# Kernel tuning notes

Measured on AMD Instinct MI355X. Metric: run time of the kernel, lower is better.

## Reference

```python
import jax, jax.numpy as jnp
import numpy as np

N = 20
DM = 128
C_CLIP = 10.0
BATCH = 16384


def setup_inputs() -> dict:
    key = jax.random.key(0)
    ks = jax.random.split(key, 9)
    s = 1.0 / np.sqrt(DM)
    inp = {
        "x": jax.random.normal(ks[0], (BATCH, N, DM), dtype=jnp.float32),
        "Wg": jax.random.uniform(ks[1], (DM, DM), jnp.float32, -s, s),
        "bg": jax.random.uniform(ks[2], (DM,), jnp.float32, -s, s),
        "Wn": jax.random.uniform(ks[3], (DM, DM), jnp.float32, -s, s),
        "bn": jax.random.uniform(ks[4], (DM,), jnp.float32, -s, s),
        "Wk": jax.random.uniform(ks[5], (DM, DM), jnp.float32, -s, s),
        "bk": jax.random.uniform(ks[6], (DM,), jnp.float32, -s, s),
        "Wq": jax.random.uniform(ks[7], (DM, DM), jnp.float32, -s, s),
        "bq": jax.random.uniform(ks[8], (DM,), jnp.float32, -s, s),
    }
    return inp


def reference(x, Wg, bg, Wn, bn, Wk, bk, Wq, bq):
    B, n, dm = x.shape
    # graph embedding: max-pool over nodes
    x_graph = jnp.max(x, axis=1)                      # [B, dm]
    lp_graph = x_graph @ Wg.T + bg                    # [B, dm]
    lp_nodes = x @ Wn.T + bn                          # [B, n, dm]
    h = lp_nodes + lp_graph[:, None, :]               # [B, n, dm]
    K = h @ Wk.T + bk                                 # [B, n, dm]
    Q = h @ Wq.T + bq                                 # [B, n, dm]
    M = jnp.einsum("bnd,bmd->bnm", K, Q) / np.float32(np.sqrt(dm))
    M_hat = C_CLIP * jnp.tanh(M) - jnp.eye(n, dtype=M.dtype) * 1e20
    # flattened (global) softmax over all n*n entries
    p = jax.nn.softmax(M_hat.reshape(B, n * n), axis=1)
    return p.reshape(B, n, n)
```

## Files before the change

kernel.cpp:

```cpp
#include <hip/hip_runtime.h>
#include <hip/hip_bf16.h>
#include <math.h>

#define DM 128
#define NN 20
#define NB 16384
#define BPB 8

#define OFF_A      0
#define OFF_AT     16384
#define OFF_WA     32768
#define OFF_WAT    49152
#define OFF_AG     65536
#define OFF_BMAT   81920
#define OFF_S1T    98304
#define OFF_S2T    114688
#define OFF_C2T    131072
#define OFF_U0     147456
#define OFF_V0     147584
#define OFF_T0     147712
#define OFF_W1     147840
#define OFF_AT0    147968
#define OFF_A0     148096
#define OFF_B0     148224
#define OFF_C1     148352
#define OFF_C00    148480
#define OFF_CBASE  148481
#define OFF_FRAGB  149504
#define OFF_FRAGS  (149504 + 8192)

#define INVS 0.08838834764831845f

typedef _Float16 h16;
typedef h16 half8 __attribute__((ext_vector_type(8)));
typedef h16 half4v __attribute__((ext_vector_type(4)));
typedef h16 half2v __attribute__((ext_vector_type(2)));
typedef float f32x4 __attribute__((ext_vector_type(4)));
typedef unsigned int uint4v __attribute__((ext_vector_type(4)));

#define MFMA16(a, b, c) __builtin_amdgcn_mfma_f32_16x16x32_f16((a), (b), (c), 0, 0, 0)

__device__ __forceinline__ int swz(int row, int col) {
    return (row * 128 + col) ^ ((row & 7) << 3);
}

__device__ __forceinline__ unsigned pkmax(unsigned a, unsigned b) {
    const half2v r = __builtin_elementwise_max(__builtin_bit_cast(half2v, a),
                                               __builtin_bit_cast(half2v, b));
    return __builtin_bit_cast(unsigned, r);
}

__device__ __forceinline__ unsigned pk2(float a, float b) {
    const half2v p = { (h16)a, (h16)b };
    return __builtin_bit_cast(unsigned, p);
}

__device__ __forceinline__ int fb_idx(int k, int j) {
    return ((j >> 4) << 11) | ((k >> 5) << 9)
         | ((((k >> 3) & 3) * 16 + (j & 15)) << 3) | (k & 7);
}

__global__ void k_prep1(const float* __restrict__ Wk, const float* __restrict__ Wq,
                        const float* __restrict__ bk, const float* __restrict__ bq,
                        const float* __restrict__ bn, const float* __restrict__ bg,
                        float* __restrict__ ws) {
    const int bx = blockIdx.x, t = threadIdx.x;
    __shared__ float sbuf[128];
    if (bx < 128) {
        sbuf[t] = Wk[t * 128 + bx];
        __syncthreads();
        float a = 0.f;
        #pragma unroll 8
        for (int d = 0; d < 128; ++d) a += sbuf[d] * Wq[d * 128 + t];
        ws[OFF_A  + bx * 128 + t] = a;
        ws[OFF_AT + t * 128 + bx] = a;
    } else {
        float u = 0.f, v = 0.f;
        #pragma unroll 8
        for (int d = 0; d < 128; ++d) {
            u += Wk[d * 128 + t] * bq[d];
            v += Wq[d * 128 + t] * bk[d];
        }
        ws[OFF_U0 + t] = u;
        ws[OFF_V0 + t] = v;
        ws[OFF_T0 + t] = bn[t] + bg[t];
        sbuf[t] = bk[t] * bq[t];
        __syncthreads();
        for (int s = 64; s > 0; s >>= 1) { if (t < s) sbuf[t] += sbuf[t + s]; __syncthreads(); }
        if (t == 0) ws[OFF_C00] = sbuf[0];
    }
}

__global__ void k_prep2(const float* __restrict__ Wn, const float* __restrict__ Wg,
                        float* __restrict__ ws) {
    const int bx = blockIdx.x, t = threadIdx.x;
    __shared__ float s1[128], s2[128];
    if (bx < 128) {
        const int r = bx;
        s1[t] = Wn[t * 128 + r];
        s2[t] = ws[OFF_A + r * 128 + t];
        __syncthreads();
        float wa = 0.f, wat = 0.f, ag = 0.f;
        #pragma unroll 4
        for (int e = 0; e < 128; ++e) {
            wa  += s1[e] * ws[OFF_A  + e * 128 + t];
            wat += s1[e] * ws[OFF_AT + e * 128 + t];
            ag  += s2[e] * Wg[e * 128 + t];
        }
        ws[OFF_WA  + r * 128 + t] = wa;
        ws[OFF_WAT + r * 128 + t] = wat;
        ws[OFF_AG  + r * 128 + t] = ag;
    } else {
        const float t0t = ws[OFF_T0 + t], u0t = ws[OFF_U0 + t], v0t = ws[OFF_V0 + t];
        float w1 = 0.f, at0 = 0.f;
        #pragma unroll 8
        for (int e = 0; e < 128; ++e) {
            const float t0e = ws[OFF_T0 + e];
            w1  += (ws[OFF_A + t * 128 + e] + ws[OFF_AT + t * 128 + e]) * t0e;
            at0 +=  ws[OFF_A + t * 128 + e] * t0e;
        }
        w1 += u0t + v0t;
        ws[OFF_W1  + t] = w1;
        ws[OFF_AT0 + t] = at0;
        s1[t] = t0t * (at0 + u0t + v0t);
        __syncthreads();
        for (int s = 64; s > 0; s >>= 1) { if (t < s) s1[t] += s1[t + s]; __syncthreads(); }
        if (t == 0) ws[OFF_CBASE] = s1[0] + ws[OFF_C00];
    }
}

__global__ void k_prep3(const float* __restrict__ Wn, const float* __restrict__ Wg,
                        float* __restrict__ ws) {
    const int bx = blockIdx.x, t = threadIdx.x;
    __shared__ float wa[128], wat[128], wgc[128];
    h16* fB = (h16*)(ws + OFF_FRAGB);
    h16* fS = (h16*)(ws + OFF_FRAGS);
    if (bx < 128) {
        const int r = bx;
        wa[t]  = ws[OFF_WA  + r * 128 + t];
        wat[t] = ws[OFF_WAT + r * 128 + t];
        wgc[t] = Wg[t * 128 + r];
        __syncthreads();
        float bm = 0.f, s1v = 0.f, s2v = 0.f, c2v = 0.f;
        #pragma unroll 4
        for (int f = 0; f < 128; ++f) {
            bm  += wa[f]  * Wn[f * 128 + t];
            s1v += wa[f]  * Wg[f * 128 + t];
            s2v += wat[f] * Wg[f * 128 + t];
            c2v += wgc[f] * ws[OFF_AG + f * 128 + t];
        }
        fB[fb_idx(r, t)]       = (h16)bm;
        fS[fb_idx(t, r)]       = (h16)s1v;
        fS[fb_idx(t, r + 128)] = (h16)s2v;
        fS[fb_idx(t, r + 256)] = (h16)c2v;
    } else {
        float a0 = 0.f, b0 = 0.f, c1 = 0.f;
        #pragma unroll 8
        for (int f = 0; f < 128; ++f) {
            a0 += ws[OFF_WA  + t * 128 + f] * ws[OFF_T0 + f] + Wn[f * 128 + t] * ws[OFF_U0 + f];
            b0 += ws[OFF_WAT + t * 128 + f] * ws[OFF_T0 + f] + Wn[f * 128 + t] * ws[OFF_V0 + f];
            c1 += Wg[f * 128 + t] * ws[OFF_W1 + f];
        }
        ws[OFF_A0 + t] = a0;
        ws[OFF_B0 + t] = b0;
        ws[OFF_C1 + t] = c1;
    }
}

__global__ __launch_bounds__(512, 4) void k_fused(const float* __restrict__ x,
                                                  const float* __restrict__ ws,
                                                  float* __restrict__ out) {
    __shared__ __align__(16) h16 xgl[BPB * 128];
    __shared__ __align__(16) h16 avhL[BPB * 2 * 128];
    __shared__ float abL[BPB][40];
    __shared__ float cpart[BPB][BPB];
    __shared__ float cbs[BPB];

    const int t = threadIdx.x, l = t & 63, w = t >> 6;
    const int lc = l & 15, lg = l >> 4;
    const int b = blockIdx.x * BPB + w;
    const half8 h8z = {};

    const float* xb = x + (size_t)b * 2560;
    half8 xa0[4], xa1[4];
    #pragma unroll
    for (int ks = 0; ks < 4; ++ks) {
        const float4 v0 = *(const float4*)(xb + lc * 128 + 32 * ks + 8 * lg);
        const float4 v1 = *(const float4*)(xb + lc * 128 + 32 * ks + 8 * lg + 4);
        xa0[ks] = (half8){ (h16)v0.x, (h16)v0.y, (h16)v0.z, (h16)v0.w,
                           (h16)v1.x, (h16)v1.y, (h16)v1.z, (h16)v1.w };
    }
    #pragma unroll
    for (int ks = 0; ks < 4; ++ks) {
        half8 v = h8z;
        if (lc < 4) {
            const float4 v0 = *(const float4*)(xb + (16 + lc) * 128 + 32 * ks + 8 * lg);
            const float4 v1 = *(const float4*)(xb + (16 + lc) * 128 + 32 * ks + 8 * lg + 4);
            v = (half8){ (h16)v0.x, (h16)v0.y, (h16)v0.z, (h16)v0.w,
                         (h16)v1.x, (h16)v1.y, (h16)v1.z, (h16)v1.w };
        }
        xa1[ks] = v;
    }

    #pragma unroll
    for (int ks = 0; ks < 4; ++ks) {
        uint4v m0 = __builtin_bit_cast(uint4v, xa0[ks]);
        uint4v m1 = __builtin_bit_cast(uint4v, xa1[ks]);
        #pragma unroll
        for (int s = 1; s < 16; s <<= 1) {
            #pragma unroll
            for (int wd = 0; wd < 4; ++wd)
                m0[wd] = pkmax(m0[wd], (unsigned)__shfl_xor((int)m0[wd], s));
        }
        #pragma unroll
        for (int s = 1; s < 4; s <<= 1) {
            #pragma unroll
            for (int wd = 0; wd < 4; ++wd)
                m1[wd] = pkmax(m1[wd], (unsigned)__shfl_xor((int)m1[wd], s));
        }
        #pragma unroll
        for (int wd = 0; wd < 4; ++wd) {
            const unsigned m1b = (unsigned)__shfl((int)m1[wd], l & 51);
            m0[wd] = pkmax(m0[wd], m1b);
        }
        if (lc == 0)
            *(half8*)(xgl + swz(w, 32 * ks + 8 * lg)) = __builtin_bit_cast(half8, m0);
    }
    __syncthreads();

    {
        const half8* fS = (const half8*)(ws + OFF_FRAGS);
        f32x4 sacc[3];
        #pragma unroll
        for (int i = 0; i < 3; ++i) sacc[i] = (f32x4){0.f, 0.f, 0.f, 0.f};
        #pragma unroll
        for (int ks = 0; ks < 4; ++ks) {
            const half8 ag = *(const half8*)(xgl + swz(lc & 7, 32 * ks + 8 * lg));
            #pragma unroll
            for (int i = 0; i < 3; ++i) {
                const int ct = w + 8 * i;
                sacc[i] = MFMA16(ag, fS[(ct * 4 + ks) * 64 + l], sacc[i]);
            }
        }
        #pragma unroll
        for (int i = 0; i < 2; ++i) {
            const int ct = w + 8 * i;
            const int v = ct >> 3, c128 = 16 * (ct & 7) + lc;
            const float bias = (v == 0) ? ws[OFF_A0 + c128] : ws[OFF_B0 + c128];
            if (lg < 2) {
                #pragma unroll
                for (int r = 0; r < 4; ++r)
                    avhL[(4 * lg + r) * 256 + v * 128 + c128] = (h16)(sacc[i][r] + bias);
            }
        }
        {
            const int j = 16 * w + lc;
            const float c1j = ws[OFF_C1 + j];
            float p[4];
            #pragma unroll
            for (int r = 0; r < 4; ++r) {
                const float xgv = (float)xgl[swz((4 * lg + r) & 7, j)];
                p[r] = (sacc[2][r] + c1j) * xgv;
            }
            #pragma unroll
            for (int r = 0; r < 4; ++r) {
                float v = p[r];
                v += __shfl_xor(v, 1); v += __shfl_xor(v, 2);
                v += __shfl_xor(v, 4); v += __shfl_xor(v, 8);
                if (lc == 0 && lg < 2) cpart[4 * lg + r][w] = v;
            }
        }
    }
    __syncthreads();
    if (t < BPB) {
        float s = ws[OFF_CBASE];
        #pragma unroll
        for (int j = 0; j < BPB; ++j) s += cpart[t][j];
        cbs[t] = s;
    }
    __syncthreads();

    half8 s8[4];
    #pragma unroll
    for (int ks = 0; ks < 4; ++ks) {
        half8 v = h8z;
        if (lc < 2) v = *(const half8*)(avhL + w * 256 + lc * 128 + 32 * ks + 8 * lg);
        s8[ks] = v;
    }
    {
        f32x4 a0c = {0.f, 0.f, 0.f, 0.f}, a1c = {0.f, 0.f, 0.f, 0.f};
        #pragma unroll
        for (int ks = 0; ks < 4; ++ks) {
            a0c = MFMA16(xa0[ks], s8[ks], a0c);
            a1c = MFMA16(xa1[ks], s8[ks], a1c);
        }
        if (lc == 0) {
            #pragma unroll
            for (int r = 0; r < 4; ++r) abL[w][4 * lg + r] = a0c[r];
            if (lg == 0) {
                #pragma unroll
                for (int r = 0; r < 4; ++r) abL[w][16 + r] = a1c[r];
            }
        }
        if (lc == 1) {
            #pragma unroll
            for (int r = 0; r < 4; ++r) abL[w][20 + 4 * lg + r] = a0c[r];
            if (lg == 0) {
                #pragma unroll
                for (int r = 0; r < 4; ++r) abL[w][36 + r] = a1c[r];
            }
        }
    }

    const half8* fB = (const half8*)(ws + OFF_FRAGB);
    f32x4 macc[2][2];
    #pragma unroll
    for (int mt = 0; mt < 2; ++mt)
        #pragma unroll
        for (int ctn = 0; ctn < 2; ++ctn) macc[mt][ctn] = (f32x4){0.f, 0.f, 0.f, 0.f};
    const bool hs = (l < 32);
    const int s1 = lc + ((l >> 4) & 1) * 32;
    const int s2 = s1 + 16;
    #pragma unroll
    for (int km = 0; km < 4; ++km) {
        unsigned P[2][2][2];
        #pragma unroll
        for (int rp = 0; rp < 2; ++rp) {
            const int rt = 2 * km + rp;
            f32x4 f0 = {0.f, 0.f, 0.f, 0.f}, f1 = {0.f, 0.f, 0.f, 0.f};
            #pragma unroll
            for (int ks = 0; ks < 4; ++ks) {
                const half8 a = fB[(rt * 4 + ks) * 64 + l];
                f0 = MFMA16(a, xa0[ks], f0);
                f1 = MFMA16(a, xa1[ks], f1);
            }
            P[rp][0][0] = pk2(f0[0], f0[1]); P[rp][0][1] = pk2(f0[2], f0[3]);
            P[rp][1][0] = pk2(f1[0], f1[1]); P[rp][1][1] = pk2(f1[2], f1[3]);
        }
        #pragma unroll
        for (int ctn = 0; ctn < 2; ++ctn) {
            const unsigned A0 = (unsigned)__shfl((int)P[0][ctn][0], s1);
            const unsigned B0 = (unsigned)__shfl((int)P[1][ctn][0], s1);
            const unsigned A1 = (unsigned)__shfl((int)P[0][ctn][1], s1);
            const unsigned B1 = (unsigned)__shfl((int)P[1][ctn][1], s1);
            const unsigned A2 = (unsigned)__shfl((int)P[0][ctn][0], s2);
            const unsigned B2 = (unsigned)__shfl((int)P[1][ctn][0], s2);
            const unsigned A3 = (unsigned)__shfl((int)P[0][ctn][1], s2);
            const unsigned B3 = (unsigned)__shfl((int)P[1][ctn][1], s2);
            const uint4v uu = { hs ? A0 : B0, hs ? A1 : B1,
                                hs ? A2 : B2, hs ? A3 : B3 };
            const half8 bX = __builtin_bit_cast(half8, uu);
            macc[0][ctn] = MFMA16(xa0[km], bX, macc[0][ctn]);
            macc[1][ctn] = MFMA16(xa1[km], bX, macc[1][ctn]);
        }
    }
    asm volatile("s_waitcnt lgkmcnt(0)" ::: "memory");

    const float cb = cbs[w];
    const float an0 = abL[w][lc];
    const float an1 = (lc < 4) ? abL[w][16 + lc] : 0.f;
    float bmv0[4], bmv1[4];
    #pragma unroll
    for (int r = 0; r < 4; ++r) {
        bmv0[r] = abL[w][20 + 4 * lg + r];
        bmv1[r] = (lg == 0) ? abL[w][36 + r] : 0.f;
    }
    float pv[2][2][4];
    float psum = 0.f;
    #pragma unroll
    for (int mt = 0; mt < 2; ++mt) {
        #pragma unroll
        for (int ctn = 0; ctn < 2; ++ctn) {
            #pragma unroll
            for (int r = 0; r < 4; ++r) {
                const int n = 16 * ctn + lc;
                const int m = 16 * mt + 4 * lg + r;
                const bool valid = (ctn == 0 || lc < 4) && (mt == 0 || lg == 0) && (n != m);
                const float Mv = (macc[mt][ctn][r] + (ctn ? an1 : an0)
                                  + (mt ? bmv1[r] : bmv0[r]) + cb) * INVS;
                const float E = __expf(2.f * Mv);
                const float e = valid ? __expf(-20.f / (E + 1.f)) : 0.f;
                pv[mt][ctn][r] = e;
                psum += e;
            }
        }
    }
    #pragma unroll
    for (int off = 32; off > 0; off >>= 1) psum += __shfl_xor(psum, off);
    const float inv = 1.f / psum;

    float* ob = out + (size_t)b * 400;
    #pragma unroll
    for (int ctn = 0; ctn < 2; ++ctn) {
        if (ctn == 0 || lc < 4) {
            const int n = 16 * ctn + lc;
            #pragma unroll
            for (int mt = 0; mt < 2; ++mt) {
                if (mt == 0 || lg == 0) {
                    const f32x4 o = { pv[mt][ctn][0] * inv, pv[mt][ctn][1] * inv,
                                      pv[mt][ctn][2] * inv, pv[mt][ctn][3] * inv };
                    *(f32x4*)(ob + n * 20 + 16 * mt + 4 * lg) = o;
                }
            }
        }
    }
}

extern "C" void kernel_launch(void* const* d_in, const int* in_sizes, int n_in,
                              void* d_out, int out_size, void* d_ws, size_t ws_size,
                              hipStream_t stream) {
    const float* x  = (const float*)d_in[0];
    const float* Wg = (const float*)d_in[1];
    const float* bg = (const float*)d_in[2];
    const float* Wn = (const float*)d_in[3];
    const float* bn = (const float*)d_in[4];
    const float* Wk = (const float*)d_in[5];
    const float* bk = (const float*)d_in[6];
    const float* Wq = (const float*)d_in[7];
    const float* bq = (const float*)d_in[8];
    float* out = (float*)d_out;
    float* ws  = (float*)d_ws;

    k_prep1<<<129, 128, 0, stream>>>(Wk, Wq, bk, bq, bn, bg, ws);
    k_prep2<<<129, 128, 0, stream>>>(Wn, Wg, ws);
    k_prep3<<<129, 128, 0, stream>>>(Wn, Wg, ws);
    k_fused<<<NB / BPB, 512, 0, stream>>>(x, ws, out);
}
```

Baseline: 119.7 us.

## Process two batches per wave and stage FRAGB weight fragments in LDS

Each block now handles 16 graphs, two per wave, which halves the grid. The shared weight fragment matrix FRAGB (32 KB of half) is copied once per block into LDS, and the per-batch MFMA loop reads it from there instead of from global memory. The graph-projection MFMA now uses all 16 rows, where before half were wasted. In exchange, register pressure rises because two batches of x fragments are held at once, and the larger LDS footprint may lower occupancy below the launch_bounds target.

Result: faster. 104.4 us (-12.8%).

```diff
diff --git a/kernel.cpp b/kernel.cpp
--- a/kernel.cpp
+++ b/kernel.cpp
@@ -5,7 +5,6 @@
 #define DM 128
 #define NN 20
 #define NB 16384
-#define BPB 8
 
 #define OFF_A      0
 #define OFF_AT     16384
@@ -170,62 +169,86 @@
 __global__ __launch_bounds__(512, 4) void k_fused(const float* __restrict__ x,
                                                   const float* __restrict__ ws,
                                                   float* __restrict__ out) {
-    __shared__ __align__(16) h16 xgl[BPB * 128];
-    __shared__ __align__(16) h16 avhL[BPB * 2 * 128];
-    __shared__ float abL[BPB][40];
-    __shared__ float cpart[BPB][BPB];
-    __shared__ float cbs[BPB];
+    __shared__ __align__(16) h16 fBl[16384];
+    __shared__ __align__(16) h16 xgl[16 * 128];
+    __shared__ __align__(16) h16 avhL[16 * 2 * 128];
+    __shared__ float abL[16][40];
+    __shared__ float cpart[16][8];
+    __shared__ float cbs[16];
 
     const int t = threadIdx.x, l = t & 63, w = t >> 6;
     const int lc = l & 15, lg = l >> 4;
-    const int b = blockIdx.x * BPB + w;
+    const int b0 = blockIdx.x * 16;
     const half8 h8z = {};
 
-    const float* xb = x + (size_t)b * 2560;
-    half8 xa0[4], xa1[4];
-    #pragma unroll
-    for (int ks = 0; ks < 4; ++ks) {
-        const float4 v0 = *(const float4*)(xb + lc * 128 + 32 * ks + 8 * lg);
-        const float4 v1 = *(const float4*)(xb + lc * 128 + 32 * ks + 8 * lg + 4);
-        xa0[ks] = (half8){ (h16)v0.x, (h16)v0.y, (h16)v0.z, (h16)v0.w,
-                           (h16)v1.x, (h16)v1.y, (h16)v1.z, (h16)v1.w };
-    }
-    #pragma unroll
-    for (int ks = 0; ks < 4; ++ks) {
-        half8 v = h8z;
-        if (lc < 4) {
-            const float4 v0 = *(const float4*)(xb + (16 + lc) * 128 + 32 * ks + 8 * lg);
-            const float4 v1 = *(const float4*)(xb + (16 + lc) * 128 + 32 * ks + 8 * lg + 4);
-            v = (half8){ (h16)v0.x, (h16)v0.y, (h16)v0.z, (h16)v0.w,
-                         (h16)v1.x, (h16)v1.y, (h16)v1.z, (h16)v1.w };
-        }
-        xa1[ks] = v;
-    }
-
-    #pragma unroll
-    for (int ks = 0; ks < 4; ++ks) {
-        uint4v m0 = __builtin_bit_cast(uint4v, xa0[ks]);
-        uint4v m1 = __builtin_bit_cast(uint4v, xa1[ks]);
-        #pragma unroll
-        for (int s = 1; s < 16; s <<= 1) {
-            #pragma unroll
-            for (int wd = 0; wd < 4; ++wd)
-                m0[wd] = pkmax(m0[wd], (unsigned)__shfl_xor((int)m0[wd], s));
-        }
-        #pragma unroll
-        for (int s = 1; s < 4; s <<= 1) {
-            #pragma unroll
-            for (int wd = 0; wd < 4; ++wd)
-                m1[wd] = pkmax(m1[wd], (unsigned)__shfl_xor((int)m1[wd], s));
-        }
-        #pragma unroll
-        for (int wd = 0; wd < 4; ++wd) {
-            const unsigned m1b = (unsigned)__shfl((int)m1[wd], l & 51);
-            m0[wd] = pkmax(m0[wd], m1b);
-        }
-        if (lc == 0)
-            *(half8*)(xgl + swz(w, 32 * ks + 8 * lg)) = __builtin_bit_cast(half8, m0);
-    }
+    {
+        const float4* src = (const float4*)(ws + OFF_FRAGB);
+        float4* dst = (float4*)fBl;
+        #pragma unroll
+        for (int i = 0; i < 4; ++i) dst[t + 512 * i] = src[t + 512 * i];
+    }
+
+    half8 xA0[4], xA1[4], xB0[4], xB1[4];
+    {
+        const float* xa = x + (size_t)(b0 + 2 * w) * 2560;
+        const float* xb = x + (size_t)(b0 + 2 * w + 1) * 2560;
+        #pragma unroll
+        for (int ks = 0; ks < 4; ++ks) {
+            const float4 a0 = *(const float4*)(xa + lc * 128 + 32 * ks + 8 * lg);
+            const float4 a1 = *(const float4*)(xa + lc * 128 + 32 * ks + 8 * lg + 4);
+            xA0[ks] = (half8){ (h16)a0.x, (h16)a0.y, (h16)a0.z, (h16)a0.w,
+                               (h16)a1.x, (h16)a1.y, (h16)a1.z, (h16)a1.w };
+            const float4 c0 = *(const float4*)(xb + lc * 128 + 32 * ks + 8 * lg);
+            const float4 c1 = *(const float4*)(xb + lc * 128 + 32 * ks + 8 * lg + 4);
+            xB0[ks] = (half8){ (h16)c0.x, (h16)c0.y, (h16)c0.z, (h16)c0.w,
+                               (h16)c1.x, (h16)c1.y, (h16)c1.z, (h16)c1.w };
+        }
+        #pragma unroll
+        for (int ks = 0; ks < 4; ++ks) {
+            half8 va = h8z, vb = h8z;
+            if (lc < 4) {
+                const float4 a0 = *(const float4*)(xa + (16 + lc) * 128 + 32 * ks + 8 * lg);
+                const float4 a1 = *(const float4*)(xa + (16 + lc) * 128 + 32 * ks + 8 * lg + 4);
+                va = (half8){ (h16)a0.x, (h16)a0.y, (h16)a0.z, (h16)a0.w,
+                              (h16)a1.x, (h16)a1.y, (h16)a1.z, (h16)a1.w };
+                const float4 c0 = *(const float4*)(xb + (16 + lc) * 128 + 32 * ks + 8 * lg);
+                const float4 c1 = *(const float4*)(xb + (16 + lc) * 128 + 32 * ks + 8 * lg + 4);
+                vb = (half8){ (h16)c0.x, (h16)c0.y, (h16)c0.z, (h16)c0.w,
+                              (h16)c1.x, (h16)c1.y, (h16)c1.z, (h16)c1.w };
+            }
+            xA1[ks] = va;
+            xB1[ks] = vb;
+        }
+    }
+
+    auto xg_store = [&](const half8 (&y0)[4], const half8 (&y1)[4], int row) {
+        #pragma unroll
+        for (int ks = 0; ks < 4; ++ks) {
+            uint4v m0 = __builtin_bit_cast(uint4v, y0[ks]);
+            uint4v m1 = __builtin_bit_cast(uint4v, y1[ks]);
+            #pragma unroll
+            for (int s = 1; s < 16; s <<= 1) {
+                #pragma unroll
+                for (int wd = 0; wd < 4; ++wd)
+                    m0[wd] = pkmax(m0[wd], (unsigned)__shfl_xor((int)m0[wd], s));
+            }
+            #pragma unroll
+            for (int s = 1; s < 4; s <<= 1) {
+                #pragma unroll
+                for (int wd = 0; wd < 4; ++wd)
+                    m1[wd] = pkmax(m1[wd], (unsigned)__shfl_xor((int)m1[wd], s));
+            }
+            #pragma unroll
+            for (int wd = 0; wd < 4; ++wd) {
+                const unsigned m1b = (unsigned)__shfl((int)m1[wd], l & 51);
+                m0[wd] = pkmax(m0[wd], m1b);
+            }
+            if (lc == 0)
+                *(half8*)(xgl + swz(row, 32 * ks + 8 * lg)) = __builtin_bit_cast(half8, m0);
+        }
+    };
+    xg_store(xA0, xA1, 2 * w);
+    xg_store(xB0, xB1, 2 * w + 1);
     __syncthreads();
 
     {
@@ -235,7 +258,7 @@
         for (int i = 0; i < 3; ++i) sacc[i] = (f32x4){0.f, 0.f, 0.f, 0.f};
         #pragma unroll
         for (int ks = 0; ks < 4; ++ks) {
-            const half8 ag = *(const half8*)(xgl + swz(lc & 7, 32 * ks + 8 * lg));
+            const half8 ag = *(const half8*)(xgl + swz(lc, 32 * ks + 8 * lg));
             #pragma unroll
             for (int i = 0; i < 3; ++i) {
                 const int ct = w + 8 * i;
@@ -247,163 +270,160 @@
             const int ct = w + 8 * i;
             const int v = ct >> 3, c128 = 16 * (ct & 7) + lc;
             const float bias = (v == 0) ? ws[OFF_A0 + c128] : ws[OFF_B0 + c128];
-            if (lg < 2) {
-                #pragma unroll
-                for (int r = 0; r < 4; ++r)
-                    avhL[(4 * lg + r) * 256 + v * 128 + c128] = (h16)(sacc[i][r] + bias);
-            }
+            #pragma unroll
+            for (int r = 0; r < 4; ++r)
+                avhL[(4 * lg + r) * 256 + v * 128 + c128] = (h16)(sacc[i][r] + bias);
         }
         {
             const int j = 16 * w + lc;
             const float c1j = ws[OFF_C1 + j];
-            float p[4];
             #pragma unroll
             for (int r = 0; r < 4; ++r) {
-                const float xgv = (float)xgl[swz((4 * lg + r) & 7, j)];
-                p[r] = (sacc[2][r] + c1j) * xgv;
-            }
-            #pragma unroll
-            for (int r = 0; r < 4; ++r) {
-                float v = p[r];
+                float v = (sacc[2][r] + c1j) * (float)xgl[swz(4 * lg + r, j)];
                 v += __shfl_xor(v, 1); v += __shfl_xor(v, 2);
                 v += __shfl_xor(v, 4); v += __shfl_xor(v, 8);
-                if (lc == 0 && lg < 2) cpart[4 * lg + r][w] = v;
+                if (lc == 0) cpart[4 * lg + r][w] = v;
             }
         }
     }
     __syncthreads();
-    if (t < BPB) {
+    if (t < 16) {
         float s = ws[OFF_CBASE];
         #pragma unroll
-        for (int j = 0; j < BPB; ++j) s += cpart[t][j];
+        for (int j = 0; j < 8; ++j) s += cpart[t][j];
         cbs[t] = s;
     }
     __syncthreads();
 
-    half8 s8[4];
-    #pragma unroll
-    for (int ks = 0; ks < 4; ++ks) {
-        half8 v = h8z;
-        if (lc < 2) v = *(const half8*)(avhL + w * 256 + lc * 128 + 32 * ks + 8 * lg);
-        s8[ks] = v;
-    }
-    {
-        f32x4 a0c = {0.f, 0.f, 0.f, 0.f}, a1c = {0.f, 0.f, 0.f, 0.f};
-        #pragma unroll
-        for (int ks = 0; ks < 4; ++ks) {
-            a0c = MFMA16(xa0[ks], s8[ks], a0c);
-            a1c = MFMA16(xa1[ks], s8[ks], a1c);
-        }
-        if (lc == 0) {
-            #pragma unroll
-            for (int r = 0; r < 4; ++r) abL[w][4 * lg + r] = a0c[r];
-            if (lg == 0) {
-                #pragma unroll
-                for (int r = 0; r < 4; ++r) abL[w][16 + r] = a1c[r];
-            }
-        }
-        if (lc == 1) {
-            #pragma unroll
-            for (int r = 0; r < 4; ++r) abL[w][20 + 4 * lg + r] = a0c[r];
-            if (lg == 0) {
-                #pragma unroll
-                for (int r = 0; r < 4; ++r) abL[w][36 + r] = a1c[r];
-            }
-        }
-    }
-
-    const half8* fB = (const half8*)(ws + OFF_FRAGB);
-    f32x4 macc[2][2];
-    #pragma unroll
-    for (int mt = 0; mt < 2; ++mt)
-        #pragma unroll
-        for (int ctn = 0; ctn < 2; ++ctn) macc[mt][ctn] = (f32x4){0.f, 0.f, 0.f, 0.f};
     const bool hs = (l < 32);
     const int s1 = lc + ((l >> 4) & 1) * 32;
     const int s2 = s1 + 16;
-    #pragma unroll
-    for (int km = 0; km < 4; ++km) {
-        unsigned P[2][2][2];
-        #pragma unroll
-        for (int rp = 0; rp < 2; ++rp) {
-            const int rt = 2 * km + rp;
-            f32x4 f0 = {0.f, 0.f, 0.f, 0.f}, f1 = {0.f, 0.f, 0.f, 0.f};
+
+    auto per_batch = [&](const half8 (&y0)[4], const half8 (&y1)[4], const int bi) {
+        half8 s8[4];
+        #pragma unroll
+        for (int ks = 0; ks < 4; ++ks) {
+            half8 v = h8z;
+            if (lc < 2) v = *(const half8*)(avhL + bi * 256 + lc * 128 + 32 * ks + 8 * lg);
+            s8[ks] = v;
+        }
+        {
+            f32x4 a0c = {0.f, 0.f, 0.f, 0.f}, a1c = {0.f, 0.f, 0.f, 0.f};
             #pragma unroll
             for (int ks = 0; ks < 4; ++ks) {
-                const half8 a = fB[(rt * 4 + ks) * 64 + l];
-                f0 = MFMA16(a, xa0[ks], f0);
-                f1 = MFMA16(a, xa1[ks], f1);
-            }
-            P[rp][0][0] = pk2(f0[0], f0[1]); P[rp][0][1] = pk2(f0[2], f0[3]);
-            P[rp][1][0] = pk2(f1[0], f1[1]); P[rp][1][1] = pk2(f1[2], f1[3]);
-        }
+                a0c = MFMA16(y0[ks], s8[ks], a0c);
+                a1c = MFMA16(y1[ks], s8[ks], a1c);
+            }
+            if (lc == 0) {
+                #pragma unroll
+                for (int r = 0; r < 4; ++r) abL[bi][4 * lg + r] = a0c[r];
+                if (lg == 0) {
+                    #pragma unroll
+                    for (int r = 0; r < 4; ++r) abL[bi][16 + r] = a1c[r];
+                }
+            }
+            if (lc == 1) {
+                #pragma unroll
+                for (int r = 0; r < 4; ++r) abL[bi][20 + 4 * lg + r] = a0c[r];
+                if (lg == 0) {
+                    #pragma unroll
+                    for (int r = 0; r < 4; ++r) abL[bi][36 + r] = a1c[r];
+                }
+            }
+        }
+
+        f32x4 macc[2][2];
+        #pragma unroll
+        for (int mt = 0; mt < 2; ++mt)
+            #pragma unroll
+            for (int ctn = 0; ctn < 2; ++ctn) macc[mt][ctn] = (f32x4){0.f, 0.f, 0.f, 0.f};
+        #pragma unroll
+        for (int km = 0; km < 4; ++km) {
+            unsigned P[2][2][2];
+            #pragma unroll
+            for (int rp = 0; rp < 2; ++rp) {
+                const int rt = 2 * km + rp;
+                f32x4 f0 = {0.f, 0.f, 0.f, 0.f}, f1 = {0.f, 0.f, 0.f, 0.f};
+                #pragma unroll
+                for (int ks = 0; ks < 4; ++ks) {
+                    const half8 a = *(const half8*)(fBl + ((rt * 4 + ks) * 64 + l) * 8);
+                    f0 = MFMA16(a, y0[ks], f0);
+                    f1 = MFMA16(a, y1[ks], f1);
+                }
+                P[rp][0][0] = pk2(f0[0], f0[1]); P[rp][0][1] = pk2(f0[2], f0[3]);
+                P[rp][1][0] = pk2(f1[0], f1[1]); P[rp][1][1] = pk2(f1[2], f1[3]);
+            }
+            #pragma unroll
+            for (int ctn = 0; ctn < 2; ++ctn) {
+                const unsigned A0 = (unsigned)__shfl((int)P[0][ctn][0], s1);
+                const unsigned B0 = (unsigned)__shfl((int)P[1][ctn][0], s1);
+                const unsigned A1 = (unsigned)__shfl((int)P[0][ctn][1], s1);
+                const unsigned B1 = (unsigned)__shfl((int)P[1][ctn][1], s1);
+                const unsigned A2 = (unsigned)__shfl((int)P[0][ctn][0], s2);
+                const unsigned B2 = (unsigned)__shfl((int)P[1][ctn][0], s2);
+                const unsigned A3 = (unsigned)__shfl((int)P[0][ctn][1], s2);
+                const unsigned B3 = (unsigned)__shfl((int)P[1][ctn][1], s2);
+                const uint4v uu = { hs ? A0 : B0, hs ? A1 : B1,
+                                    hs ? A2 : B2, hs ? A3 : B3 };
+                const half8 bX = __builtin_bit_cast(half8, uu);
+                macc[0][ctn] = MFMA16(y0[km], bX, macc[0][ctn]);
+                macc[1][ctn] = MFMA16(y1[km], bX, macc[1][ctn]);
+            }
+        }
+        asm volatile("s_waitcnt lgkmcnt(0)" ::: "memory");
+
+        const float cb = cbs[bi];
+        const float an0 = abL[bi][lc];
+        const float an1 = (lc < 4) ? abL[bi][16 + lc] : 0.f;
+        float bmv0[4], bmv1[4];
+        #pragma unroll
+        for (int r = 0; r < 4; ++r) {
+            bmv0[r] = abL[bi][20 + 4 * lg + r];
+            bmv1[r] = (lg == 0) ? abL[bi][36 + r] : 0.f;
+        }
+        float pv[2][2][4];
+        float psum = 0.f;
+        #pragma unroll
+        for (int mt = 0; mt < 2; ++mt) {
+            #pragma unroll
+            for (int ctn = 0; ctn < 2; ++ctn) {
+                #pragma unroll
+                for (int r = 0; r < 4; ++r) {
+                    const int n = 16 * ctn + lc;
+                    const int m = 16 * mt + 4 * lg + r;
+                    const bool valid = (ctn == 0 || lc < 4) && (mt == 0 || lg == 0) && (n != m);
+                    const float Mv = (macc[mt][ctn][r] + (ctn ? an1 : an0)
+                                      + (mt ? bmv1[r] : bmv0[r]) + cb) * INVS;
+                    const float E = __expf(2.f * Mv);
+                    const float e = valid ? __expf(-20.f / (E + 1.f)) : 0.f;
+                    pv[mt][ctn][r] = e;
+                    psum += e;
+                }
+            }
+        }
+        #pragma unroll
+        for (int off = 32; off > 0; off >>= 1) psum += __shfl_xor(psum, off);
+        const float inv = 1.f / psum;
+
+        float* ob = out + (size_t)(b0 + bi) * 400;
         #pragma unroll
         for (int ctn = 0; ctn < 2; ++ctn) {
-            const unsigned A0 = (unsigned)__shfl((int)P[0][ctn][0], s1);
-            const unsigned B0 = (unsigned)__shfl((int)P[1][ctn][0], s1);
-            const unsigned A1 = (unsigned)__shfl((int)P[0][ctn][1], s1);
-            const unsigned B1 = (unsigned)__shfl((int)P[1][ctn][1], s1);
-            const unsigned A2 = (unsigned)__shfl((int)P[0][ctn][0], s2);
-            const unsigned B2 = (unsigned)__shfl((int)P[1][ctn][0], s2);
-            const unsigned A3 = (unsigned)__shfl((int)P[0][ctn][1], s2);
-            const unsigned B3 = (unsigned)__shfl((int)P[1][ctn][1], s2);
-            const uint4v uu = { hs ? A0 : B0, hs ? A1 : B1,
-                                hs ? A2 : B2, hs ? A3 : B3 };
-            const half8 bX = __builtin_bit_cast(half8, uu);
-            macc[0][ctn] = MFMA16(xa0[km], bX, macc[0][ctn]);
-            macc[1][ctn] = MFMA16(xa1[km], bX, macc[1][ctn]);
-        }
-    }
-    asm volatile("s_waitcnt lgkmcnt(0)" ::: "memory");
-
-    const float cb = cbs[w];
-    const float an0 = abL[w][lc];
-    const float an1 = (lc < 4) ? abL[w][16 + lc] : 0.f;
-    float bmv0[4], bmv1[4];
-    #pragma unroll
-    for (int r = 0; r < 4; ++r) {
-        bmv0[r] = abL[w][20 + 4 * lg + r];
-        bmv1[r] = (lg == 0) ? abL[w][36 + r] : 0.f;
-    }
-    float pv[2][2][4];
-    float psum = 0.f;
-    #pragma unroll
-    for (int mt = 0; mt < 2; ++mt) {
-        #pragma unroll
-        for (int ctn = 0; ctn < 2; ++ctn) {
-            #pragma unroll
-            for (int r = 0; r < 4; ++r) {
+            if (ctn == 0 || lc < 4) {
                 const int n = 16 * ctn + lc;
-                const int m = 16 * mt + 4 * lg + r;
-                const bool valid = (ctn == 0 || lc < 4) && (mt == 0 || lg == 0) && (n != m);
-                const float Mv = (macc[mt][ctn][r] + (ctn ? an1 : an0)
-                                  + (mt ? bmv1[r] : bmv0[r]) + cb) * INVS;
-                const float E = __expf(2.f * Mv);
-                const float e = valid ? __expf(-20.f / (E + 1.f)) : 0.f;
-                pv[mt][ctn][r] = e;
-                psum += e;
-            }
-        }
-    }
-    #pragma unroll
-    for (int off = 32; off > 0; off >>= 1) psum += __shfl_xor(psum, off);
-    const float inv = 1.f / psum;
-
-    float* ob = out + (size_t)b * 400;
-    #pragma unroll
-    for (int ctn = 0; ctn < 2; ++ctn) {
-        if (ctn == 0 || lc < 4) {
-            const int n = 16 * ctn + lc;
-            #pragma unroll
-            for (int mt = 0; mt < 2; ++mt) {
-                if (mt == 0 || lg == 0) {
-                    const f32x4 o = { pv[mt][ctn][0] * inv, pv[mt][ctn][1] * inv,
-                                      pv[mt][ctn][2] * inv, pv[mt][ctn][3] * inv };
-                    *(f32x4*)(ob + n * 20 + 16 * mt + 4 * lg) = o;
+                #pragma unroll
+                for (int mt = 0; mt < 2; ++mt) {
+                    if (mt == 0 || lg == 0) {
+                        const f32x4 o = { pv[mt][ctn][0] * inv, pv[mt][ctn][1] * inv,
+                                          pv[mt][ctn][2] * inv, pv[mt][ctn][3] * inv };
+                        *(f32x4*)(ob + n * 20 + 16 * mt + 4 * lg) = o;
+                    }
                 }
             }
         }
-    }
+    };
+
+    per_batch(xA0, xA1, 2 * w);
+    per_batch(xB0, xB1, 2 * w + 1);
 }
 
 extern "C" void kernel_launch(void* const* d_in, const int* in_sizes, int n_in,
@@ -424,5 +444,5 @@
     k_prep1<<<129, 128, 0, stream>>>(Wk, Wq, bk, bq, bn, bg, ws);
     k_prep2<<<129, 128, 0, stream>>>(Wn, Wg, ws);
     k_prep3<<<129, 128, 0, stream>>>(Wn, Wg, ws);
-    k_fused<<<NB / BPB, 512, 0, stream>>>(x, ws, out);
-}
+    k_fused<<<NB / 16, 512, 0, stream>>>(x, ws, out);
+}
```
